# Optimization experiments

Hardware: AMD Instinct MI355X
Metric: run time of the kernel (lower is better)

Reference implementation:

```python
import jax, jax.numpy as jnp
import numpy as np

B, D, L, H = 2048, 64, 64, 512  # batch, in_dim, latent_space, hidden


def setup_inputs() -> dict:
    key = jax.random.key(0)
    ks = jax.random.split(key, 12)
    inp = {
        "x": jax.random.normal(ks[0], (B, D), jnp.float32),
        "koopman": jax.random.normal(ks[1], (B, L, D), jnp.float32),
    }
    dims = [(L, H), (H, H), (H, H), (H, D)]
    k = 2
    for pfx in ("s", "t"):
        for j, (fi, fo) in enumerate(dims):
            inp[f"{pfx}W{j+1}"] = jax.random.normal(ks[k], (fi, fo), jnp.float32) / np.sqrt(fi).astype(np.float32)
            inp[f"{pfx}b{j+1}"] = jnp.zeros((fo,), jnp.float32)
            k += 1
    return inp


def _mlp(z, W1, b1, W2, b2, W3, b3, W4, b4):
    h = jnp.tanh(z @ W1 + b1)
    h = jnp.tanh(h @ W2 + b2)
    h = jnp.tanh(h @ W3 + b3)
    return h @ W4 + b4


def reference(x, koopman,
              sW1, sb1, sW2, sb2, sW3, sb3, sW4, sb4,
              tW1, tb1, tW2, tb2, tW3, tb3, tW4, tb4):
    # koopman: (B, L, D) -> z: (B, D, L); column i of the torch loop is z[:, i, :]
    z = jnp.swapaxes(koopman, 1, 2)
    s = _mlp(z, sW1, sb1, sW2, sb2, sW3, sb3, sW4, sb4)  # (B, D, D)
    t = _mlp(z, tW1, tb1, tW2, tb2, tW3, tb3, tW4, tb4)  # (B, D, D)
    # loop kept only output column i for input column i -> diagonal over last two dims
    ds = jnp.diagonal(s, axis1=1, axis2=2)  # (B, D)
    dt = jnp.diagonal(t, axis1=1, axis2=2)  # (B, D)
    return (x - dt) * jnp.exp(-ds)
```

## Files before the change

### kernel.cpp

```cpp
#include <hip/hip_runtime.h>


typedef _Float16 f16;
typedef _Float16 f16x8 __attribute__((ext_vector_type(8)));
typedef float f32x16 __attribute__((ext_vector_type(16)));

#define WPACK_PER_NET 589824
#define OFF_W1 0
#define OFF_W2 32768
#define OFF_W3 294912
#define OFF_W4T 557056
#define WPACK_BYTES (2u * WPACK_PER_NET * sizeof(f16))

__global__ void pack_weights(const float* __restrict__ sW1, const float* __restrict__ sW2,
                             const float* __restrict__ sW3, const float* __restrict__ sW4,
                             const float* __restrict__ tW1, const float* __restrict__ tW2,
                             const float* __restrict__ tW3, const float* __restrict__ tW4,
                             f16* __restrict__ dst) {
  int idx8 = (blockIdx.x * 256 + threadIdx.x) * 8;
  if (idx8 >= 2 * WPACK_PER_NET) return;
  int net = idx8 >= WPACK_PER_NET;
  int f = idx8 - net * WPACK_PER_NET;
  const float* W1 = net ? tW1 : sW1;
  const float* W2 = net ? tW2 : sW2;
  const float* W3 = net ? tW3 : sW3;
  const float* W4 = net ? tW4 : sW4;
  f16x8 o;
  if (f < OFF_W2) {
    int lane = (f >> 3) & 63, ctg = (f >> 9) & 15, ks = f >> 13;
    int r0 = ks * 16 + (lane >> 5) * 8, c = ctg * 32 + (lane & 31);
#pragma unroll
    for (int j = 0; j < 8; j++) o[j] = (f16)W1[(r0 + j) * 512 + c];
  } else if (f < OFF_W3) {
    int f2 = f - OFF_W2;
    int lane = (f2 >> 3) & 63, ctg = (f2 >> 9) & 15, ks = f2 >> 13;
    int r0 = ks * 16 + (lane >> 5) * 8, c = ctg * 32 + (lane & 31);
#pragma unroll
    for (int j = 0; j < 8; j++) o[j] = (f16)W2[(r0 + j) * 512 + c];
  } else if (f < OFF_W4T) {
    int f3 = f - OFF_W3;
    int lane = (f3 >> 3) & 63, ctg = (f3 >> 9) & 15, ks = f3 >> 13;
    int r0 = ks * 16 + (lane >> 5) * 8, c = ctg * 32 + (lane & 31);
#pragma unroll
    for (int j = 0; j < 8; j++) o[j] = (f16)W3[(r0 + j) * 512 + c];
  } else {
    int f4 = f - OFF_W4T;
    int i = f4 >> 9, k0 = f4 & 511;
#pragma unroll
    for (int j = 0; j < 8; j++) o[j] = (f16)W4[(k0 + j) * 64 + i];
  }
  *(f16x8*)(dst + net * WPACK_PER_NET + f) = o;
}

__device__ __forceinline__ int aidx(int m, int k) {
  return ((k >> 4) * 2 + (m >> 5)) * 512 + ((m & 31) + 32 * ((k >> 3) & 1)) * 8 + (k & 7);
}

__device__ __forceinline__ float fast_tanh(float x) {
  float e = __expf(x + x);
  return fmaf(-2.0f, __builtin_amdgcn_rcpf(e + 1.0f), 1.0f);
}

template <bool PACKED>
__device__ __forceinline__ void load_b(const f16* __restrict__ Wblk,
                                       const float* __restrict__ Wraw,
                                       int ks, int wave, int lane, f16x8* bdst) {
  if (PACKED) {
#pragma unroll
    for (int ct = 0; ct < 2; ct++)
      bdst[ct] = *(const f16x8*)(Wblk + ((ks * 16 + wave * 2 + ct) * 64 + lane) * 8);
  } else {
    int r0 = ks * 16 + (lane >> 5) * 8;
    int n0 = wave * 64 + (lane & 31);
#pragma unroll
    for (int ct = 0; ct < 2; ct++) {
      f16x8 v;
#pragma unroll
      for (int j = 0; j < 8; j++) v[j] = (f16)Wraw[(r0 + j) * 512 + n0 + ct * 32];
      bdst[ct] = v;
    }
  }
}

template <int NS, bool PACKED, bool ALIASED>
__device__ __forceinline__ void mlp_layer(const f16* __restrict__ Wblk,
                                          const float* __restrict__ Wraw,
                                          const float* __restrict__ bias,
                                          const f16* Asrc, f16* Hout,
                                          int wave, int lane, int sbase) {
  f32x16 acc[2][2];
#pragma unroll
  for (int ct = 0; ct < 2; ct++) {
    float bv = bias[wave * 64 + ct * 32 + (lane & 31)];
#pragma unroll
    for (int mt = 0; mt < 2; mt++)
#pragma unroll
      for (int e = 0; e < 16; e++) acc[mt][ct][e] = bv;
  }

  f16x8 bb[2][2];
  load_b<PACKED>(Wblk, Wraw, 0, wave, lane, bb[0]);
#pragma unroll
  for (int ks = 0; ks < NS; ks++) {
    if (ks + 1 < NS) load_b<PACKED>(Wblk, Wraw, ks + 1, wave, lane, bb[(ks + 1) & 1]);
    const f16* ab = Asrc + ks * 1024 + lane * 8;
    f16x8 a0 = *(const f16x8*)ab;
    f16x8 a1 = *(const f16x8*)(ab + 512);
#pragma unroll
    for (int ct = 0; ct < 2; ct++) {
      acc[0][ct] = __builtin_amdgcn_mfma_f32_32x32x16_f16(a0, bb[ks & 1][ct],
                                                          acc[0][ct], 0, 0, 0);
      acc[1][ct] = __builtin_amdgcn_mfma_f32_32x32x16_f16(a1, bb[ks & 1][ct],
                                                          acc[1][ct], 0, 0, 0);
    }
  }
  if (ALIASED) __syncthreads();

  f16* hb = Hout + sbase;
#pragma unroll
  for (int mt = 0; mt < 2; mt++)
#pragma unroll
    for (int ct = 0; ct < 2; ct++)
#pragma unroll
      for (int reg = 0; reg < 16; reg++)
        hb[ct * 2048 + mt * 512 + (reg >> 2) * 64 + (reg & 3) * 8] =
            (f16)fast_tanh(acc[mt][ct][reg]);
  __syncthreads();
}

template <bool PACKED>
__global__ __launch_bounds__(512, 4) void decoder_main(
    const float* __restrict__ x, const float* __restrict__ koop,
    const f16* __restrict__ wpack,
    const float* __restrict__ sW1, const float* __restrict__ sW2,
    const float* __restrict__ sW3, const float* __restrict__ sW4,
    const float* __restrict__ tW1, const float* __restrict__ tW2,
    const float* __restrict__ tW3, const float* __restrict__ tW4,
    const float* __restrict__ sb1, const float* __restrict__ sb2,
    const float* __restrict__ sb3, const float* __restrict__ sb4,
    const float* __restrict__ tb1, const float* __restrict__ tb2,
    const float* __restrict__ tb3, const float* __restrict__ tb4,
    float* __restrict__ out) {
  __shared__ __align__(16) f16 ZA[4096];
  __shared__ __align__(16) f16 HA[32768];
  __shared__ float redBuf[2][64];

  const int b = blockIdx.x;
  const int t = threadIdx.x;
  const int wave = t >> 6, lane = t & 63;
  const int sbase = wave * 4096 + ((lane >> 4) & 1) * 1024 +
                    ((lane >> 3) & 1) * 256 + (lane >> 5) * 32 + (lane & 7);

  const float* kb = koop + b * 4096;
#pragma unroll
  for (int i = 0; i < 8; i++) {
    int flat = t + 512 * i;
    ZA[aidx(flat & 63, flat >> 6)] = (f16)kb[flat];
  }
  __syncthreads();

  for (int net = 0; net < 2; net++) {
    const f16* wb = PACKED ? (wpack + net * WPACK_PER_NET) : (const f16*)0;
    const float* W1 = net ? tW1 : sW1;
    const float* W2 = net ? tW2 : sW2;
    const float* W3 = net ? tW3 : sW3;
    const float* W4 = net ? tW4 : sW4;
    const float* b1 = net ? tb1 : sb1;
    const float* b2 = net ? tb2 : sb2;
    const float* b3 = net ? tb3 : sb3;
    const float* b4 = net ? tb4 : sb4;
    mlp_layer<4, PACKED, false>(PACKED ? wb + OFF_W1 : 0, W1, b1, ZA, HA,
                                wave, lane, sbase);
    mlp_layer<32, PACKED, true>(PACKED ? wb + OFF_W2 : 0, W2, b2, HA, HA,
                                wave, lane, sbase);
    mlp_layer<32, PACKED, true>(PACKED ? wb + OFF_W3 : 0, W3, b3, HA, HA,
                                wave, lane, sbase);

    int i = t >> 3, sub = t & 7;
    float p = 0.f;
#pragma unroll
    for (int q = 0; q < 8; q++) {
      int k0 = sub * 64 + q * 8;
      f16x8 hv = *(const f16x8*)&HA[aidx(i, k0)];
      if (PACKED) {
        f16x8 wv = *(const f16x8*)&wb[OFF_W4T + i * 512 + k0];
#pragma unroll
        for (int j = 0; j < 8; j++) p += (float)hv[j] * (float)wv[j];
      } else {
#pragma unroll
        for (int j = 0; j < 8; j++) p += (float)hv[j] * W4[(k0 + j) * 64 + i];
      }
    }
    p += __shfl_down(p, 4, 8);
    p += __shfl_down(p, 2, 8);
    p += __shfl_down(p, 1, 8);
    if (sub == 0) redBuf[net][i] = p + b4[i];
    __syncthreads();
  }

  if (t < 64) {
    out[b * 64 + t] = (x[b * 64 + t] - redBuf[1][t]) * __expf(-redBuf[0][t]);
  }
}

extern "C" void kernel_launch(void* const* d_in, const int* in_sizes, int n_in,
                              void* d_out, int out_size, void* d_ws, size_t ws_size,
                              hipStream_t stream) {
  const float* x    = (const float*)d_in[0];
  const float* koop = (const float*)d_in[1];
  const float* sW1 = (const float*)d_in[2];  const float* sb1 = (const float*)d_in[3];
  const float* sW2 = (const float*)d_in[4];  const float* sb2 = (const float*)d_in[5];
  const float* sW3 = (const float*)d_in[6];  const float* sb3 = (const float*)d_in[7];
  const float* sW4 = (const float*)d_in[8];  const float* sb4 = (const float*)d_in[9];
  const float* tW1 = (const float*)d_in[10]; const float* tb1 = (const float*)d_in[11];
  const float* tW2 = (const float*)d_in[12]; const float* tb2 = (const float*)d_in[13];
  const float* tW3 = (const float*)d_in[14]; const float* tb3 = (const float*)d_in[15];
  const float* tW4 = (const float*)d_in[16]; const float* tb4 = (const float*)d_in[17];
  float* out = (float*)d_out;

  if (ws_size >= (size_t)WPACK_BYTES) {
    f16* wpack = (f16*)d_ws;
    pack_weights<<<576, 256, 0, stream>>>(sW1, sW2, sW3, sW4, tW1, tW2, tW3, tW4, wpack);
    decoder_main<true><<<2048, 512, 0, stream>>>(
        x, koop, wpack, sW1, sW2, sW3, sW4, tW1, tW2, tW3, tW4,
        sb1, sb2, sb3, sb4, tb1, tb2, tb3, tb4, out);
  } else {
    decoder_main<false><<<2048, 512, 0, stream>>>(
        x, koop, (const f16*)0, sW1, sW2, sW3, sW4, tW1, tW2, tW3, tW4,
        sb1, sb2, sb3, sb4, tb1, tb2, tb3, tb4, out);
  }
}
```

Before: 455.5 us.

## Swizzle LDS activation layout to avoid bank conflicts and restructure final-layer dot product

```diff
diff --git a/kernel.cpp b/kernel.cpp
--- a/kernel.cpp
+++ b/kernel.cpp
@@ -56,6 +56,10 @@
   return ((k >> 4) * 2 + (m >> 5)) * 512 + ((m & 31) + 32 * ((k >> 3) & 1)) * 8 + (k & 7);
 }
 
+__device__ __forceinline__ int swz(int e) {
+  return e ^ (((e >> 8) & 1) << 3) ^ (((e >> 10) & 1) << 4);
+}
+
 __device__ __forceinline__ float fast_tanh(float x) {
   float e = __expf(x + x);
   return fmaf(-2.0f, __builtin_amdgcn_rcpf(e + 1.0f), 1.0f);
@@ -87,7 +91,8 @@
                                           const float* __restrict__ Wraw,
                                           const float* __restrict__ bias,
                                           const f16* Asrc, f16* Hout,
-                                          int wave, int lane, int sbase) {
+                                          int wave, int lane, int sbase,
+                                          int lane8s, int lane_m) {
   f32x16 acc[2][2];
 #pragma unroll
   for (int ct = 0; ct < 2; ct++) {
@@ -98,12 +103,15 @@
       for (int e = 0; e < 16; e++) acc[mt][ct][e] = bv;
   }
 
+  const f16* abE = Asrc + lane8s;
+  const f16* abO = Asrc + (lane8s ^ 16);
+
   f16x8 bb[2][2];
   load_b<PACKED>(Wblk, Wraw, 0, wave, lane, bb[0]);
 #pragma unroll
   for (int ks = 0; ks < NS; ks++) {
     if (ks + 1 < NS) load_b<PACKED>(Wblk, Wraw, ks + 1, wave, lane, bb[(ks + 1) & 1]);
-    const f16* ab = Asrc + ks * 1024 + lane * 8;
+    const f16* ab = ((ks & 1) ? abO : abE) + ks * 1024;
     f16x8 a0 = *(const f16x8*)ab;
     f16x8 a1 = *(const f16x8*)(ab + 512);
 #pragma unroll
@@ -116,15 +124,18 @@
   }
   if (ALIASED) __syncthreads();
 
-  f16* hb = Hout + sbase;
-#pragma unroll
-  for (int mt = 0; mt < 2; mt++)
-#pragma unroll
-    for (int ct = 0; ct < 2; ct++)
-#pragma unroll
-      for (int reg = 0; reg < 16; reg++)
-        hb[ct * 2048 + mt * 512 + (reg >> 2) * 64 + (reg & 3) * 8] =
-            (f16)fast_tanh(acc[mt][ct][reg]);
+#pragma unroll
+  for (int rr = 0; rr < 4; rr++) {
+    f16* hb = Hout + sbase + ((rr ^ lane_m) << 3);
+#pragma unroll
+    for (int mt = 0; mt < 2; mt++)
+#pragma unroll
+      for (int ct = 0; ct < 2; ct++)
+#pragma unroll
+        for (int rq = 0; rq < 4; rq++)
+          hb[ct * 2048 + mt * 512 + rq * 64] =
+              (f16)fast_tanh(acc[mt][ct][rq * 4 + rr]);
+  }
   __syncthreads();
 }
 
@@ -143,6 +154,7 @@
     float* __restrict__ out) {
   __shared__ __align__(16) f16 ZA[4096];
   __shared__ __align__(16) f16 HA[32768];
+  __shared__ float pp[512];
   __shared__ float redBuf[2][64];
 
   const int b = blockIdx.x;
@@ -150,12 +162,14 @@
   const int wave = t >> 6, lane = t & 63;
   const int sbase = wave * 4096 + ((lane >> 4) & 1) * 1024 +
                     ((lane >> 3) & 1) * 256 + (lane >> 5) * 32 + (lane & 7);
+  const int lane8s = (lane * 8) ^ (((lane >> 5) & 1) << 3);
+  const int lane_m = ((lane >> 3) & 1) | (((lane >> 4) & 1) << 1);
 
   const float* kb = koop + b * 4096;
 #pragma unroll
   for (int i = 0; i < 8; i++) {
     int flat = t + 512 * i;
-    ZA[aidx(flat & 63, flat >> 6)] = (f16)kb[flat];
+    ZA[swz(aidx(flat & 63, flat >> 6))] = (f16)kb[flat];
   }
   __syncthreads();
 
@@ -170,31 +184,32 @@
     const float* b3 = net ? tb3 : sb3;
     const float* b4 = net ? tb4 : sb4;
     mlp_layer<4, PACKED, false>(PACKED ? wb + OFF_W1 : 0, W1, b1, ZA, HA,
-                                wave, lane, sbase);
+                                wave, lane, sbase, lane8s, lane_m);
     mlp_layer<32, PACKED, true>(PACKED ? wb + OFF_W2 : 0, W2, b2, HA, HA,
-                                wave, lane, sbase);
+                                wave, lane, sbase, lane8s, lane_m);
     mlp_layer<32, PACKED, true>(PACKED ? wb + OFF_W3 : 0, W3, b3, HA, HA,
-                                wave, lane, sbase);
-
-    int i = t >> 3, sub = t & 7;
-    float p = 0.f;
-#pragma unroll
-    for (int q = 0; q < 8; q++) {
-      int k0 = sub * 64 + q * 8;
-      f16x8 hv = *(const f16x8*)&HA[aidx(i, k0)];
-      if (PACKED) {
-        f16x8 wv = *(const f16x8*)&wb[OFF_W4T + i * 512 + k0];
-#pragma unroll
-        for (int j = 0; j < 8; j++) p += (float)hv[j] * (float)wv[j];
-      } else {
-#pragma unroll
-        for (int j = 0; j < 8; j++) p += (float)hv[j] * W4[(k0 + j) * 64 + i];
+                                wave, lane, sbase, lane8s, lane_m);
+
+    {
+      int i = lane, oct = wave;
+      float p = 0.f;
+#pragma unroll
+      for (int q = 0; q < 8; q++) {
+        int k0 = oct * 64 + q * 8;
+        f16x8 hv = *(const f16x8*)&HA[swz(aidx(i, k0))];
+#pragma unroll
+        for (int j = 0; j < 8; j++)
+          p += (float)hv[j] * W4[(k0 + j) * 64 + i];
       }
-    }
-    p += __shfl_down(p, 4, 8);
-    p += __shfl_down(p, 2, 8);
-    p += __shfl_down(p, 1, 8);
-    if (sub == 0) redBuf[net][i] = p + b4[i];
+      pp[oct * 64 + i] = p;
+    }
+    __syncthreads();
+    if (t < 64) {
+      float s = b4[t];
+#pragma unroll
+      for (int o = 0; o < 8; o++) s += pp[o * 64 + t];
+      redBuf[net][t] = s;
+    }
     __syncthreads();
   }
 
```

Result: no change. 462.0 us (+1.4%).
